# Performance work log

Hardware: AMD Instinct MI355X
Metric: run time of the kernel (lower is better)

The kernel has to match this reference:

```python
import jax, jax.numpy as jnp
import numpy as np

EPS = 1e-9
ALPHA = 1.0
BETA = 6.0
TOPK = 13
NUM_CLASSES = 80


def _make_boxes(key, shape, img=640.0, wh_min=8.0, wh_max=128.0):
    k1, k2 = jax.random.split(key)
    cxy = jax.random.uniform(k1, shape[:-1] + (2,)) * img
    wh = wh_min + jax.random.uniform(k2, shape[:-1] + (2,)) * (wh_max - wh_min)
    return jnp.concatenate([cxy - wh / 2, cxy + wh / 2], axis=-1)


def setup_inputs() -> dict:
    key = jax.random.key(0)
    ks = jax.random.split(key, 5)
    B, N, C, M = 16, 8400, NUM_CLASSES, 64
    pd_scores = jax.random.normal(ks[0], (B, N, C), dtype=jnp.float32)  # logits
    pd_bboxes = _make_boxes(ks[1], (B, N, 4))
    anc_points = jax.random.uniform(ks[2], (N, 2)) * 640.0
    gt_labels = jax.random.randint(ks[3], (B, M, 1), 0, C).astype(jnp.int64)
    gt_bboxes = _make_boxes(ks[4], (B, M, 4), wh_min=16.0, wh_max=256.0)
    mask_gt = jnp.ones((B, M, 1), dtype=jnp.float32)
    return {"pd_scores": pd_scores, "pd_bboxes": pd_bboxes, "anc_points": anc_points,
            "gt_labels": gt_labels, "gt_bboxes": gt_bboxes, "mask_gt": mask_gt}


def _pairwise_iou(gt_bboxes, pd_bboxes):
    # gt: (B,M,4), pd: (B,N,4) -> (B,M,N)
    a1 = gt_bboxes[:, :, None, :2]
    a2 = gt_bboxes[:, :, None, 2:]
    b1 = pd_bboxes[:, None, :, :2]
    b2 = pd_bboxes[:, None, :, 2:]
    inter = jnp.clip(jnp.minimum(a2, b2) - jnp.maximum(a1, b1), 0.0).prod(-1)
    area_a = (a2 - a1).prod(-1)
    area_b = (b2 - b1).prod(-1)
    return inter / jnp.maximum(area_a + area_b - inter, EPS)


def _tal_assign(pd_scores, pd_bboxes, anc_points, gt_labels, gt_bboxes, mask_gt):
    B, N, C = pd_scores.shape
    M = gt_labels.shape[1]
    ps = jax.nn.sigmoid(pd_scores)  # input_is_logits=True
    mask_gt_bool = mask_gt[..., 0] > 0.5  # (B,M)

    # centers-in-boxes mask (B,M,N)
    xy = anc_points[None, None, :, :]
    lt = gt_bboxes[:, :, None, :2]
    rb = gt_bboxes[:, :, None, 2:]
    deltas = jnp.concatenate([xy - lt, rb - xy], axis=-1)  # (B,M,N,4)
    mask_in_gts = deltas.min(-1) > EPS
    valid = mask_in_gts & mask_gt_bool[:, :, None]

    # alignment metric: score(gt class)^alpha * IoU^beta, zero outside valid
    gt_ids = jnp.clip(gt_labels[..., 0], 0)  # (B,M)
    scores_t = jnp.swapaxes(ps, 1, 2)  # (B,C,N)
    bbox_scores = jnp.take_along_axis(scores_t, gt_ids[:, :, None], axis=1)  # (B,M,N)
    ious = _pairwise_iou(gt_bboxes, pd_bboxes)
    ious = jnp.where(valid, ious, 0.0)
    align = jnp.where(valid, (bbox_scores ** ALPHA) * (ious ** BETA), 0.0)

    # top-k anchors per GT along anchor dim
    topv, topi = jax.lax.top_k(align, TOPK)  # (B,M,K)
    sel = (topv > EPS) & mask_gt_bool[:, :, None]
    bi = jnp.arange(B)[:, None, None]
    mi = jnp.arange(M)[None, :, None]
    cnt = jnp.zeros((B, M, N), jnp.int32).at[bi, mi, topi].add(sel.astype(jnp.int32))
    topk_mask = cnt > 0
    mask_pos = (topk_mask & valid).astype(jnp.float32)  # (B,M,N)

    # resolve anchors assigned to multiple GTs: keep highest IoU GT
    fg = mask_pos.sum(axis=1)  # (B,N)
    multi = (fg > 1)[:, None, :]  # (B,1,N)
    best_gt = jnp.argmax(ious, axis=1)  # (B,N)
    is_max = jnp.swapaxes(jax.nn.one_hot(best_gt, M, dtype=mask_pos.dtype), 1, 2)  # (B,M,N)
    mask_pos = jnp.where(multi, is_max, mask_pos)
    fg_mask = mask_pos.sum(axis=1)  # (B,N)
    tgt_gt_idx = jnp.argmax(mask_pos, axis=1)  # (B,N)

    # gather targets
    target_labels = jnp.take_along_axis(gt_labels[..., 0], tgt_gt_idx, axis=1)  # (B,N)
    target_bboxes = jnp.take_along_axis(gt_bboxes, tgt_gt_idx[..., None], axis=1)  # (B,N,4)

    # normalized classification targets
    align = align * mask_pos
    max_align = align.max(axis=1, keepdims=True) + EPS  # (B,1,N)
    per_anchor = (align / max_align * (ious * mask_pos)).sum(axis=1)  # (B,N)
    onehot = jax.nn.one_hot(target_labels, C, dtype=jnp.float32)
    cls_targets = onehot * per_anchor[..., None]  # (B,N,C)
    return target_labels, target_bboxes, cls_targets, fg_mask > 0, tgt_gt_idx


def reference(pd_scores, pd_bboxes, anc_points, gt_labels, gt_bboxes, mask_gt):
    return _tal_assign(pd_scores, pd_bboxes, anc_points, gt_labels, gt_bboxes, mask_gt)
```

## Files before the change

### kernel.cpp

```cpp
#include <hip/hip_runtime.h>
#include <math.h>

#define BB 16
#define NN 8400
#define CC 80
#define MM 64
#define KTOP 13
#define FEPS 1e-9f
#define CAP 2048
#define WSEG 512
#define RPW 8

#define OFF_O1 134400
#define OFF_O2 672000
#define OFF_O3 11424000
#define OFF_O4 11558400
#define SCR_OFF 10348800

__device__ __forceinline__ float iou_pair(const float4 g, const float4 p) {
    float ix1 = fmaxf(g.x, p.x);
    float iy1 = fmaxf(g.y, p.y);
    float ix2 = fminf(g.z, p.z);
    float iy2 = fminf(g.w, p.w);
    float iw = fmaxf(ix2 - ix1, 0.0f);
    float ih = fmaxf(iy2 - iy1, 0.0f);
    float inter = iw * ih;
    float aa = (g.z - g.x) * (g.w - g.y);
    float ab = (p.z - p.x) * (p.w - p.y);
    float uni = fmaxf(aa + ab - inter, FEPS);
    return inter / uni;
}

__global__ __launch_bounds__(256) void k_zero_scratch(int* __restrict__ p, int n)
{
    int i = blockIdx.x * 256 + threadIdx.x;
    if (i < n) p[i] = 0;
}

__global__ __launch_bounds__(256) void k_select(
    const float* __restrict__ pd_scores, const float* __restrict__ pd_bboxes,
    const float* __restrict__ anc, const int* __restrict__ gt_labels,
    const float* __restrict__ gt_bboxes, const float* __restrict__ mask_gt,
    int* __restrict__ cntb, int* __restrict__ mselb, float* __restrict__ aselb)
{
    const int bm = blockIdx.x;
    const int b = bm >> 6, m = bm & 63;
    const int tid = threadIdx.x;
    const int lane = tid & 63;
    const int wid = tid >> 6;

    __shared__ unsigned long long k64[CAP];
    __shared__ unsigned short nnidx[CAP];
    __shared__ unsigned long long cand[64];
    __shared__ int scnt;

    const float4 g = *(const float4*)&gt_bboxes[(size_t)bm * 4];
    const int lab  = gt_labels[bm];
    const int labc = lab > 0 ? lab : 0;
    const bool mgb = mask_gt[bm] > 0.5f;
    const unsigned epskey = __float_as_uint(FEPS);

    if (tid == 0) scnt = 0;
    __syncthreads();

    const float4* anc4 = (const float4*)anc;
    for (int it = 0; it < 17; ++it) {
        int q = it * 256 + tid;
        bool vA = false, vB = false;
        if (q < 4200 && mgb) {
            float4 av = anc4[q];
            {
                float d1 = av.x - g.x, d2 = av.y - g.y;
                float d3 = g.z - av.x, d4 = g.w - av.y;
                vA = fminf(fminf(d1, d2), fminf(d3, d4)) > FEPS;
            }
            {
                float d1 = av.z - g.x, d2 = av.w - g.y;
                float d3 = g.z - av.z, d4 = g.w - av.w;
                vB = fminf(fminf(d1, d2), fminf(d3, d4)) > FEPS;
            }
        }
        unsigned long long balA = __ballot(vA);
        unsigned long long balB = __ballot(vB);
        if (balA | balB) {
            int cA = __popcll(balA);
            int base = 0;
            if (lane == 0) base = atomicAdd(&scnt, cA + __popcll(balB));
            base = __shfl(base, 0, 64);
            unsigned long long below = (1ull << lane) - 1ull;
            if (vA) {
                int s = base + __popcll(balA & below);
                if (s < CAP) nnidx[s] = (unsigned short)(2 * q);
            }
            if (vB) {
                int s = base + cA + __popcll(balB & below);
                if (s < CAP) nnidx[s] = (unsigned short)(2 * q + 1);
            }
        }
    }
    __syncthreads();
    const int count = min(scnt, CAP);

    const float* srow = pd_scores + (size_t)b * NN * CC + labc;
    const float* pbb  = pd_bboxes + (size_t)b * NN * 4;
    for (int i = tid; i < count; i += 256) {
        int n = nnidx[i];
        float4 p = *(const float4*)&pbb[(size_t)n * 4];
        float io = iou_pair(g, p);
        float x = srow[(size_t)n * CC];
        float s = 1.0f / (1.0f + expf(-x));
        float i2 = io * io;
        unsigned key = __float_as_uint(s * (i2 * i2 * i2));
        k64[i] = ((unsigned long long)key << 32) | (unsigned)(NN - n);
    }
    __syncthreads();

    {
        const int sbase = wid * WSEG;
        unsigned long long e[RPW];
        #pragma unroll
        for (int j = 0; j < RPW; ++j) {
            int i = sbase + lane + j * 64;
            e[j] = (i < count) ? k64[i] : 0ull;
        }
        unsigned long long lm = 0ull;
        #pragma unroll
        for (int j = 0; j < RPW; ++j) if (e[j] > lm) lm = e[j];

        unsigned long long winv = 0ull;
        for (int r = 0; r < KTOP; ++r) {
            unsigned long long bv = lm;
            #pragma unroll
            for (int off = 32; off > 0; off >>= 1) {
                unsigned long long ov = __shfl_xor(bv, off, 64);
                if (ov > bv) bv = ov;
            }
            if ((unsigned)(bv >> 32) <= epskey) break;
            if (lane == r) winv = bv;
            if (lm == bv) {
                #pragma unroll
                for (int j = 0; j < RPW; ++j) if (e[j] == bv) e[j] = 0ull;
                lm = 0ull;
                #pragma unroll
                for (int j = 0; j < RPW; ++j) if (e[j] > lm) lm = e[j];
            }
        }
        if (lane < KTOP) cand[wid * KTOP + lane] = winv;
        if (wid == 0 && lane >= 4 * KTOP) cand[lane] = 0ull;
    }
    __syncthreads();

    if (wid == 0) {
        unsigned long long v = cand[lane];
        unsigned long long winv = 0ull;
        for (int r = 0; r < KTOP; ++r) {
            unsigned long long bv = v;
            #pragma unroll
            for (int off = 32; off > 0; off >>= 1) {
                unsigned long long ov = __shfl_xor(bv, off, 64);
                if (ov > bv) bv = ov;
            }
            if ((unsigned)(bv >> 32) <= epskey) break;
            if (lane == r) winv = bv;
            if (v == bv) v = 0ull;
        }
        if (lane < KTOP) {
            unsigned hk = (unsigned)(winv >> 32);
            if (hk > epskey) {
                int n = NN - (int)(winv & 0xFFFFFFFFull);
                int ai = b * NN + n;
                atomicAdd(&cntb[ai], 1);
                atomicAdd(&mselb[ai], m);
                atomicAdd(&aselb[ai], __uint_as_float(hk));
            }
        }
    }
}

__global__ __launch_bounds__(256) void k_assign(
    const float* __restrict__ pd_scores, const float* __restrict__ pd_bboxes,
    const float* __restrict__ anc, const int* __restrict__ gt_labels,
    const float* __restrict__ gt_bboxes, const float* __restrict__ mask_gt,
    const int* __restrict__ cntb, const int* __restrict__ mselb,
    const float* __restrict__ aselb,
    float* __restrict__ out0, float* __restrict__ out1,
    float* __restrict__ out3, float* __restrict__ out4,
    float* __restrict__ perb)
{
    const int b = blockIdx.y;
    const int n = blockIdx.x * 256 + threadIdx.x;

    __shared__ float4 gtb[MM];
    __shared__ int    labS[MM];
    __shared__ float  mgS[MM];
    if (threadIdx.x < MM) {
        int m = threadIdx.x;
        gtb[m]  = *(const float4*)&gt_bboxes[(size_t)(b * MM + m) * 4];
        labS[m] = gt_labels[b * MM + m];
        mgS[m]  = mask_gt[b * MM + m];
    }
    __syncthreads();
    if (n >= NN) return;

    const size_t idx = (size_t)b * NN + n;
    const int cnt = cntb[idx];

    float per = 0.0f, fg = 0.0f;
    int mstar = 0;

    if (cnt > 0) {
        fg = 1.0f;
        const float4 p = *(const float4*)&pd_bboxes[idx * 4];
        if (cnt == 1) {
            mstar = mselb[idx];
            float a = aselb[idx];
            float io = iou_pair(gtb[mstar], p);
            per = a / (a + FEPS) * io;
        } else {
            float2 a2 = *(const float2*)&anc[2 * n];
            float bestI = -1.0f; int bestM = 0;
            for (int m = 0; m < MM; ++m) {
                float4 gg = gtb[m];
                float d1 = a2.x - gg.x, d2 = a2.y - gg.y;
                float d3 = gg.z - a2.x, d4 = gg.w - a2.y;
                bool valid = (fminf(fminf(d1, d2), fminf(d3, d4)) > FEPS) &&
                             (mgS[m] > 0.5f);
                float io = valid ? iou_pair(gg, p) : 0.0f;
                if (io > bestI) { bestI = io; bestM = m; }
            }
            mstar = bestM;
            float io = bestI;
            int lb = labS[mstar]; int lbc = lb > 0 ? lb : 0;
            float x = pd_scores[idx * CC + lbc];
            float s = 1.0f / (1.0f + expf(-x));
            float i2 = io * io;
            float a = s * (i2 * i2 * i2);
            per = a / (a + FEPS) * io;
        }
    }

    out0[idx] = (float)labS[mstar];
    ((float4*)out1)[idx] = gtb[mstar];
    out3[idx] = fg;
    out4[idx] = (float)mstar;
    perb[idx] = per;
}

__global__ __launch_bounds__(256) void k_cls(
    const float* __restrict__ out0, const float* __restrict__ perb,
    float4* __restrict__ cls4)
{
    int i = blockIdx.x * 256 + threadIdx.x;
    if (i >= BB * NN * CC / 4) return;
    int row = i / 20;
    int c4 = (i - row * 20) * 4;
    int lab = (int)out0[row];
    float per = perb[row];
    int d = lab - c4;
    float4 v;
    v.x = (d == 0) ? per : 0.0f;
    v.y = (d == 1) ? per : 0.0f;
    v.z = (d == 2) ? per : 0.0f;
    v.w = (d == 3) ? per : 0.0f;
    cls4[i] = v;
}

extern "C" void kernel_launch(void* const* d_in, const int* in_sizes, int n_in,
                              void* d_out, int out_size, void* d_ws, size_t ws_size,
                              hipStream_t stream) {
    const float* pd_scores = (const float*)d_in[0];
    const float* pd_bboxes = (const float*)d_in[1];
    const float* anc       = (const float*)d_in[2];
    const int*   gt_labels = (const int*)d_in[3];
    const float* gt_bboxes = (const float*)d_in[4];
    const float* mask_gt   = (const float*)d_in[5];

    float* out  = (float*)d_out;
    float* out0 = out;
    float* out1 = out + OFF_O1;
    float* out2 = out + OFF_O2;
    float* out3 = out + OFF_O3;
    float* out4 = out + OFF_O4;

    float* scr   = out2 + SCR_OFF;
    int*   cntb  = (int*)scr;
    int*   mselb = (int*)(scr + 134400);
    float* aselb = scr + 268800;
    float* perb  = (float*)d_ws;

    k_zero_scratch<<<dim3((403200 + 255) / 256), dim3(256), 0, stream>>>(
        (int*)scr, 403200);

    k_select<<<dim3(BB * MM), dim3(256), 0, stream>>>(
        pd_scores, pd_bboxes, anc, gt_labels, gt_bboxes, mask_gt,
        cntb, mselb, aselb);

    k_assign<<<dim3((NN + 255) / 256, BB), dim3(256), 0, stream>>>(
        pd_scores, pd_bboxes, anc, gt_labels, gt_bboxes, mask_gt,
        cntb, mselb, aselb, out0, out1, out3, out4, perb);

    const int n4 = (BB * NN * CC) / 4;
    k_cls<<<dim3((n4 + 255) / 256), dim3(256), 0, stream>>>(out0, perb, (float4*)out2);
}
```

Measured before the change: 61.58 us.

## Split in-box candidate scan into anchor-parallel kernel and add nontemporal cls stores

The per-GT scan over all 8400 anchors inside k_select is replaced by a separate k_inbox kernel. Each thread there tests one anchor against all 64 GTs and appends the anchor to per-GT candidate lists in global scratch using atomics. k_topk then reads only the compacted list and keeps the keys in registers instead of shared memory, which removes the redundant anchor reads each GT block used to do. The cls output writes switch to nontemporal stores. The cost is an extra kernel launch, global atomics, and scratch traffic, and candidate order inside each list is now nondeterministic, though ties are broken by anchor index in the key.

```diff
diff --git a/kernel.cpp b/kernel.cpp
--- a/kernel.cpp
+++ b/kernel.cpp
@@ -8,14 +8,17 @@
 #define KTOP 13
 #define FEPS 1e-9f
 #define CAP 2048
-#define WSEG 512
 #define RPW 8
+
+typedef float floatx4 __attribute__((ext_vector_type(4)));
 
 #define OFF_O1 134400
 #define OFF_O2 672000
 #define OFF_O3 11424000
 #define OFF_O4 11558400
-#define SCR_OFF 10348800
+#define CCNT_OFF 9299200
+#define CAND_OFF 9300224
+#define SCR_OFF  10348800
 
 __device__ __forceinline__ float iou_pair(const float4 g, const float4 p) {
     float ix1 = fmaxf(g.x, p.x);
@@ -31,16 +34,72 @@
     return inter / uni;
 }
 
-__global__ __launch_bounds__(256) void k_zero_scratch(int* __restrict__ p, int n)
+__global__ __launch_bounds__(256) void k_zero2(int* __restrict__ ccnt,
+                                               int* __restrict__ scr)
 {
     int i = blockIdx.x * 256 + threadIdx.x;
-    if (i < n) p[i] = 0;
-}
-
-__global__ __launch_bounds__(256) void k_select(
+    if (i < 1024) ccnt[i] = 0;
+    else if (i < 1024 + 403200) scr[i - 1024] = 0;
+}
+
+__global__ __launch_bounds__(256) void k_inbox(
+    const float* __restrict__ anc, const float* __restrict__ gt_bboxes,
+    const float* __restrict__ mask_gt,
+    int* __restrict__ ccnt, unsigned short* __restrict__ cand)
+{
+    const int b = blockIdx.y;
+    const int n = blockIdx.x * 256 + threadIdx.x;
+    const int tid = threadIdx.x;
+
+    __shared__ float4 gtb[MM];
+    __shared__ int hcnt[MM];
+    __shared__ int gbase[MM];
+
+    if (tid < MM) {
+        float4 g = *(const float4*)&gt_bboxes[(size_t)(b * MM + tid) * 4];
+        if (mask_gt[b * MM + tid] <= 0.5f)
+            g = make_float4(1e30f, 1e30f, -1e30f, -1e30f);
+        gtb[tid] = g;
+        hcnt[tid] = 0;
+    }
+    __syncthreads();
+
+    float ax = 0.0f, ay = 0.0f;
+    const bool inb = n < NN;
+    if (inb) { float2 a2 = *(const float2*)&anc[2 * n]; ax = a2.x; ay = a2.y; }
+
+    unsigned long long mask = 0ull;
+    #pragma unroll 8
+    for (int m = 0; m < MM; ++m) {
+        float4 g = gtb[m];
+        float d1 = ax - g.x, d2 = ay - g.y, d3 = g.z - ax, d4 = g.w - ay;
+        if (inb && fminf(fminf(d1, d2), fminf(d3, d4)) > FEPS)
+            mask |= 1ull << m;
+    }
+
+    unsigned long long t = mask;
+    while (t) { int m = __ffsll(t) - 1; t &= t - 1; atomicAdd(&hcnt[m], 1); }
+    __syncthreads();
+
+    if (tid < MM && hcnt[tid] > 0) {
+        gbase[tid] = atomicAdd(&ccnt[b * MM + tid], hcnt[tid]);
+        hcnt[tid] = 0;
+    }
+    __syncthreads();
+
+    t = mask;
+    while (t) {
+        int m = __ffsll(t) - 1; t &= t - 1;
+        int slot = gbase[m] + atomicAdd(&hcnt[m], 1);
+        if (slot < CAP)
+            cand[(size_t)(b * MM + m) * CAP + slot] = (unsigned short)n;
+    }
+}
+
+__global__ __launch_bounds__(256) void k_topk(
     const float* __restrict__ pd_scores, const float* __restrict__ pd_bboxes,
-    const float* __restrict__ anc, const int* __restrict__ gt_labels,
-    const float* __restrict__ gt_bboxes, const float* __restrict__ mask_gt,
+    const int* __restrict__ gt_labels, const float* __restrict__ gt_bboxes,
+    const int* __restrict__ ccnt, const unsigned short* __restrict__ cand,
     int* __restrict__ cntb, int* __restrict__ mselb, float* __restrict__ aselb)
 {
     const int bm = blockIdx.x;
@@ -49,80 +108,36 @@
     const int lane = tid & 63;
     const int wid = tid >> 6;
 
-    __shared__ unsigned long long k64[CAP];
-    __shared__ unsigned short nnidx[CAP];
-    __shared__ unsigned long long cand[64];
-    __shared__ int scnt;
+    __shared__ unsigned long long cmerge[64];
 
     const float4 g = *(const float4*)&gt_bboxes[(size_t)bm * 4];
     const int lab  = gt_labels[bm];
     const int labc = lab > 0 ? lab : 0;
-    const bool mgb = mask_gt[bm] > 0.5f;
     const unsigned epskey = __float_as_uint(FEPS);
-
-    if (tid == 0) scnt = 0;
-    __syncthreads();
-
-    const float4* anc4 = (const float4*)anc;
-    for (int it = 0; it < 17; ++it) {
-        int q = it * 256 + tid;
-        bool vA = false, vB = false;
-        if (q < 4200 && mgb) {
-            float4 av = anc4[q];
-            {
-                float d1 = av.x - g.x, d2 = av.y - g.y;
-                float d3 = g.z - av.x, d4 = g.w - av.y;
-                vA = fminf(fminf(d1, d2), fminf(d3, d4)) > FEPS;
-            }
-            {
-                float d1 = av.z - g.x, d2 = av.w - g.y;
-                float d3 = g.z - av.z, d4 = g.w - av.w;
-                vB = fminf(fminf(d1, d2), fminf(d3, d4)) > FEPS;
-            }
-        }
-        unsigned long long balA = __ballot(vA);
-        unsigned long long balB = __ballot(vB);
-        if (balA | balB) {
-            int cA = __popcll(balA);
-            int base = 0;
-            if (lane == 0) base = atomicAdd(&scnt, cA + __popcll(balB));
-            base = __shfl(base, 0, 64);
-            unsigned long long below = (1ull << lane) - 1ull;
-            if (vA) {
-                int s = base + __popcll(balA & below);
-                if (s < CAP) nnidx[s] = (unsigned short)(2 * q);
-            }
-            if (vB) {
-                int s = base + cA + __popcll(balB & below);
-                if (s < CAP) nnidx[s] = (unsigned short)(2 * q + 1);
-            }
-        }
-    }
-    __syncthreads();
-    const int count = min(scnt, CAP);
-
+    const int count = min(ccnt[bm], CAP);
+    const unsigned short* list = cand + (size_t)bm * CAP;
     const float* srow = pd_scores + (size_t)b * NN * CC + labc;
     const float* pbb  = pd_bboxes + (size_t)b * NN * 4;
-    for (int i = tid; i < count; i += 256) {
-        int n = nnidx[i];
-        float4 p = *(const float4*)&pbb[(size_t)n * 4];
-        float io = iou_pair(g, p);
-        float x = srow[(size_t)n * CC];
-        float s = 1.0f / (1.0f + expf(-x));
-        float i2 = io * io;
-        unsigned key = __float_as_uint(s * (i2 * i2 * i2));
-        k64[i] = ((unsigned long long)key << 32) | (unsigned)(NN - n);
-    }
-    __syncthreads();
+
+    unsigned long long e[RPW];
+    #pragma unroll
+    for (int j = 0; j < RPW; ++j) {
+        int i = tid + j * 256;
+        unsigned long long v = 0ull;
+        if (i < count) {
+            int n = list[i];
+            float4 p = *(const float4*)&pbb[(size_t)n * 4];
+            float io = iou_pair(g, p);
+            float x = srow[(size_t)n * CC];
+            float s = 1.0f / (1.0f + expf(-x));
+            float i2 = io * io;
+            unsigned key = __float_as_uint(s * (i2 * i2 * i2));
+            v = ((unsigned long long)key << 32) | (unsigned)(NN - n);
+        }
+        e[j] = v;
+    }
 
     {
-        const int sbase = wid * WSEG;
-        unsigned long long e[RPW];
-        #pragma unroll
-        for (int j = 0; j < RPW; ++j) {
-            int i = sbase + lane + j * 64;
-            e[j] = (i < count) ? k64[i] : 0ull;
-        }
         unsigned long long lm = 0ull;
         #pragma unroll
         for (int j = 0; j < RPW; ++j) if (e[j] > lm) lm = e[j];
@@ -145,13 +160,13 @@
                 for (int j = 0; j < RPW; ++j) if (e[j] > lm) lm = e[j];
             }
         }
-        if (lane < KTOP) cand[wid * KTOP + lane] = winv;
-        if (wid == 0 && lane >= 4 * KTOP) cand[lane] = 0ull;
+        if (lane < KTOP) cmerge[wid * KTOP + lane] = winv;
+        if (wid == 0 && lane >= 4 * KTOP) cmerge[lane] = 0ull;
     }
     __syncthreads();
 
     if (wid == 0) {
-        unsigned long long v = cand[lane];
+        unsigned long long v = cmerge[lane];
         unsigned long long winv = 0ull;
         for (int r = 0; r < KTOP; ++r) {
             unsigned long long bv = v;
@@ -248,7 +263,7 @@
 
 __global__ __launch_bounds__(256) void k_cls(
     const float* __restrict__ out0, const float* __restrict__ perb,
-    float4* __restrict__ cls4)
+    floatx4* __restrict__ cls4)
 {
     int i = blockIdx.x * 256 + threadIdx.x;
     if (i >= BB * NN * CC / 4) return;
@@ -257,12 +272,12 @@
     int lab = (int)out0[row];
     float per = perb[row];
     int d = lab - c4;
-    float4 v;
+    floatx4 v;
     v.x = (d == 0) ? per : 0.0f;
     v.y = (d == 1) ? per : 0.0f;
     v.z = (d == 2) ? per : 0.0f;
     v.w = (d == 3) ? per : 0.0f;
-    cls4[i] = v;
+    __builtin_nontemporal_store(v, &cls4[i]);
 }
 
 extern "C" void kernel_launch(void* const* d_in, const int* in_sizes, int n_in,
@@ -282,17 +297,22 @@
     float* out3 = out + OFF_O3;
     float* out4 = out + OFF_O4;
 
-    float* scr   = out2 + SCR_OFF;
-    int*   cntb  = (int*)scr;
-    int*   mselb = (int*)(scr + 134400);
-    float* aselb = scr + 268800;
-    float* perb  = (float*)d_ws;
-
-    k_zero_scratch<<<dim3((403200 + 255) / 256), dim3(256), 0, stream>>>(
-        (int*)scr, 403200);
-
-    k_select<<<dim3(BB * MM), dim3(256), 0, stream>>>(
-        pd_scores, pd_bboxes, anc, gt_labels, gt_bboxes, mask_gt,
+    int*            ccnt  = (int*)(out2 + CCNT_OFF);
+    unsigned short* cand  = (unsigned short*)(out2 + CAND_OFF);
+    float*          scr   = out2 + SCR_OFF;
+    int*            cntb  = (int*)scr;
+    int*            mselb = (int*)(scr + 134400);
+    float*          aselb = scr + 268800;
+    float*          perb  = (float*)d_ws;
+
+    k_zero2<<<dim3((1024 + 403200 + 255) / 256), dim3(256), 0, stream>>>(
+        ccnt, (int*)scr);
+
+    k_inbox<<<dim3((NN + 255) / 256, BB), dim3(256), 0, stream>>>(
+        anc, gt_bboxes, mask_gt, ccnt, cand);
+
+    k_topk<<<dim3(BB * MM), dim3(256), 0, stream>>>(
+        pd_scores, pd_bboxes, gt_labels, gt_bboxes, ccnt, cand,
         cntb, mselb, aselb);
 
     k_assign<<<dim3((NN + 255) / 256, BB), dim3(256), 0, stream>>>(
@@ -300,5 +320,5 @@
         cntb, mselb, aselb, out0, out1, out3, out4, perb);
 
     const int n4 = (BB * NN * CC) / 4;
-    k_cls<<<dim3((n4 + 255) / 256), dim3(256), 0, stream>>>(out0, perb, (float4*)out2);
-}
+    k_cls<<<dim3((n4 + 255) / 256), dim3(256), 0, stream>>>(out0, perb, (floatx4*)out2);
+}
```

Result: slower. 64.65 us (+5.0%).
